# Performance work log

Hardware: AMD Instinct MI355X
Metric: run time of the kernel (lower is better)

Reference implementation:

```python
import jax, jax.numpy as jnp
from jax import lax
import numpy as np

B, T, F, H, O = 4096, 2048, 8, 32, 8


def setup_inputs() -> dict:
    key = jax.random.key(0)
    k = jax.random.split(key, 7)
    s = 1.0 / np.sqrt(H).astype(np.float32)  # torch RNN/Linear init bound
    x = jax.random.normal(k[0], (B, T, F), dtype=jnp.float32)
    W_ih = jax.random.uniform(k[1], (H, F), minval=-s, maxval=s, dtype=jnp.float32)
    W_hh = jax.random.uniform(k[2], (H, H), minval=-s, maxval=s, dtype=jnp.float32)
    b_ih = jax.random.uniform(k[3], (H,), minval=-s, maxval=s, dtype=jnp.float32)
    b_hh = jax.random.uniform(k[4], (H,), minval=-s, maxval=s, dtype=jnp.float32)
    W_out = jax.random.uniform(k[5], (O, H), minval=-s, maxval=s, dtype=jnp.float32)
    b_out = jax.random.uniform(k[6], (O,), minval=-s, maxval=s, dtype=jnp.float32)
    return {"x": x, "W_ih": W_ih, "W_hh": W_hh, "b_ih": b_ih, "b_hh": b_hh,
            "W_out": W_out, "b_out": b_out}


def reference(x, W_ih, W_hh, b_ih, b_hh, W_out, b_out):
    # Precompute input projection for all timesteps: [B, T, H]
    xp = jnp.einsum('btf,hf->bth', x, W_ih) + b_ih + b_hh
    h0 = jnp.zeros((x.shape[0], W_hh.shape[0]), dtype=x.dtype)

    def step(h, xt):  # xt: [B, H]
        h = jnp.tanh(xt + h @ W_hh.T)
        return h, None

    h_final, _ = lax.scan(step, h0, jnp.swapaxes(xp, 0, 1))  # scan over T
    # torch returns out(h) with h of shape [num_layers=1, B, H]
    y = h_final @ W_out.T + b_out  # [B, O]
    return y[None]  # [1, B, O]
```

## Files before the change

kernel.cpp:

```cpp
#include <hip/hip_runtime.h>


typedef float v2f __attribute__((ext_vector_type(2)));

static constexpr int T_STEPS = 2048;
static constexpr int FDIM    = 8;
static constexpr int HDIM    = 32;
static constexpr int ODIM    = 8;
static constexpr int WAVES_PER_BLOCK = 4;
static constexpr int GROUP   = 4;
static constexpr int NGROUP  = T_STEPS / GROUP;

__global__ __launch_bounds__(256, 4) void rnn_scan_kernel(
    const float* __restrict__ x,
    const float* __restrict__ W_ih,
    const float* __restrict__ W_hh,
    const float* __restrict__ b_ih,
    const float* __restrict__ b_hh,
    const float* __restrict__ W_out,
    const float* __restrict__ b_out,
    float* __restrict__ out)
{
    const float K = 2.8853900817779268f;
    const int tid  = threadIdx.x;
    const int lane = tid & 63;
    const int wave = tid >> 6;
    const int q    = lane & 31;
    const int half = lane >> 5;
    const long long b = (long long)blockIdx.x * WAVES_PER_BLOCK + wave;

    __shared__ float hsh[WAVES_PER_BLOCK][HDIM];

    v2f wh2[8];
    const float* whr = W_hh + q * HDIM + half * 16;
#pragma unroll
    for (int i = 0; i < 8; ++i) {
        v2f w; w[0] = whr[2 * i] * K; w[1] = whr[2 * i + 1] * K; wh2[i] = w;
    }
    v2f wi2[2];
    const float* wir = W_ih + q * FDIM + half * 4;
    {
        v2f w; w[0] = wir[0] * K; w[1] = wir[1] * K; wi2[0] = w;
        w[0] = wir[2] * K; w[1] = wir[3] * K; wi2[1] = w;
    }
    const float bias = half ? 0.0f : (b_ih[q] + b_hh[q]) * K;

    const int paddr = ((lane ^ 32) & 63) * 4;

    hsh[wave][q] = 0.0f;

    const float4* xq = reinterpret_cast<const float4*>(x + (size_t)b * T_STEPS * FDIM);
    const float4* hp = reinterpret_cast<const float4*>(&hsh[wave][half * 16]);
    float* hw = &hsh[wave][q];

    float4 cx0 = xq[0 + half], cx1 = xq[2 + half],
           cx2 = xq[4 + half], cx3 = xq[6 + half];

    for (int g = 0; g < NGROUP; ++g) {
        const int nb = ((g + 1 < NGROUP) ? (g + 1) : g) * (2 * GROUP);
        float4 nx0 = xq[nb + 0 + half], nx1 = xq[nb + 2 + half],
               nx2 = xq[nb + 4 + half], nx3 = xq[nb + 6 + half];
        asm volatile("" ::: "memory");

#define STEP(xr)                                                               \
        {                                                                      \
            float4 g0 = hp[0], g1 = hp[1], g2 = hp[2], g3 = hp[3];             \
            v2f a0; a0[0] = bias; a0[1] = 0.0f;                                \
            v2f a1; a1[0] = 0.0f; a1[1] = 0.0f;                                \
            v2f t2;                                                            \
            t2[0] = xr.x; t2[1] = xr.y;  a0 += wi2[0] * t2;                    \
            t2[0] = xr.z; t2[1] = xr.w;  a1 += wi2[1] * t2;                    \
            t2[0] = g0.x; t2[1] = g0.y;  a0 += wh2[0] * t2;                    \
            t2[0] = g0.z; t2[1] = g0.w;  a1 += wh2[1] * t2;                    \
            t2[0] = g1.x; t2[1] = g1.y;  a0 += wh2[2] * t2;                    \
            t2[0] = g1.z; t2[1] = g1.w;  a1 += wh2[3] * t2;                    \
            t2[0] = g2.x; t2[1] = g2.y;  a0 += wh2[4] * t2;                    \
            t2[0] = g2.z; t2[1] = g2.w;  a1 += wh2[5] * t2;                    \
            t2[0] = g3.x; t2[1] = g3.y;  a0 += wh2[6] * t2;                    \
            t2[0] = g3.z; t2[1] = g3.w;  a1 += wh2[7] * t2;                    \
            v2f as = a0 + a1;                                                  \
            float part = as[0] + as[1];                                        \
            float oth  = __int_as_float(__builtin_amdgcn_ds_bpermute(          \
                             paddr, __float_as_int(part)));                    \
            float s = part + oth;                                              \
            float e = __builtin_amdgcn_exp2f(s);                               \
            float r = __builtin_amdgcn_rcpf(e + 1.0f);                         \
            *hw = fmaf(-2.0f, r, 1.0f);                                        \
        }

        STEP(cx0) STEP(cx1) STEP(cx2) STEP(cx3)
#undef STEP

        cx0 = nx0; cx1 = nx1; cx2 = nx2; cx3 = nx3;
    }

    __syncthreads();
    if (tid < WAVES_PER_BLOCK * ODIM) {
        const int r = tid >> 3;
        const int o = tid & 7;
        float acc = b_out[o];
#pragma unroll
        for (int j = 0; j < HDIM; ++j)
            acc = fmaf(hsh[r][j], W_out[o * HDIM + j], acc);
        out[((long long)blockIdx.x * WAVES_PER_BLOCK + r) * ODIM + o] = acc;
    }
}

extern "C" void kernel_launch(void* const* d_in, const int* in_sizes, int n_in,
                              void* d_out, int out_size, void* d_ws, size_t ws_size,
                              hipStream_t stream) {
    const float* x     = (const float*)d_in[0];
    const float* W_ih  = (const float*)d_in[1];
    const float* W_hh  = (const float*)d_in[2];
    const float* b_ih  = (const float*)d_in[3];
    const float* b_hh  = (const float*)d_in[4];
    const float* W_out = (const float*)d_in[5];
    const float* b_out = (const float*)d_in[6];

    const int B = in_sizes[0] / (T_STEPS * FDIM);
    const int grid = B / WAVES_PER_BLOCK;

    rnn_scan_kernel<<<grid, 256, 0, stream>>>(
        x, W_ih, W_hh, b_ih, b_hh, W_out, b_out, (float*)d_out);
}
```

Before: 742.7 us.

## Map one batch row per half-wave, full 32-wide dot per lane

Each half-wave now owns one batch row, so every lane computes the full 32-element recurrent dot product instead of splitting it across two lanes. This removes the per-step ds_bpermute cross-lane reduction and doubles the rows per block to 8. The 8-element x rows are loaded through double-buffered register groups, and shared-memory rows are padded to a stride of 36 to spread LDS banks. Each lane now does twice the FMAs per step and holds more registers, with launch bounds reduced to 2 blocks per CU.

```diff
diff --git a/kernel.cpp b/kernel.cpp
--- a/kernel.cpp
+++ b/kernel.cpp
@@ -7,11 +7,12 @@
 static constexpr int FDIM    = 8;
 static constexpr int HDIM    = 32;
 static constexpr int ODIM    = 8;
-static constexpr int WAVES_PER_BLOCK = 4;
+static constexpr int ROWS_PER_BLOCK = 8;
 static constexpr int GROUP   = 4;
 static constexpr int NGROUP  = T_STEPS / GROUP;
+static constexpr int LSTR    = 36;
 
-__global__ __launch_bounds__(256, 4) void rnn_scan_kernel(
+__global__ __launch_bounds__(256, 2) void rnn_scan_kernel(
     const float* __restrict__ x,
     const float* __restrict__ W_ih,
     const float* __restrict__ W_hh,
@@ -26,83 +27,104 @@
     const int lane = tid & 63;
     const int wave = tid >> 6;
     const int q    = lane & 31;
-    const int half = lane >> 5;
-    const long long b = (long long)blockIdx.x * WAVES_PER_BLOCK + wave;
+    const int sub  = lane >> 5;
+    const int r    = wave * 2 + sub;
+    const long long b = (long long)blockIdx.x * ROWS_PER_BLOCK + r;
 
-    __shared__ float hsh[WAVES_PER_BLOCK][HDIM];
+    __shared__ float hsh[ROWS_PER_BLOCK][LSTR];
 
-    v2f wh2[8];
-    const float* whr = W_hh + q * HDIM + half * 16;
+    v2f wh[16];
+    const float* whr = W_hh + q * HDIM;
 #pragma unroll
-    for (int i = 0; i < 8; ++i) {
-        v2f w; w[0] = whr[2 * i] * K; w[1] = whr[2 * i + 1] * K; wh2[i] = w;
+    for (int i = 0; i < 16; ++i) {
+        v2f w; w[0] = whr[2 * i] * K; w[1] = whr[2 * i + 1] * K; wh[i] = w;
     }
-    v2f wi2[2];
-    const float* wir = W_ih + q * FDIM + half * 4;
-    {
-        v2f w; w[0] = wir[0] * K; w[1] = wir[1] * K; wi2[0] = w;
-        w[0] = wir[2] * K; w[1] = wir[3] * K; wi2[1] = w;
+    v2f wiv[4];
+    const float* wir = W_ih + q * FDIM;
+#pragma unroll
+    for (int i = 0; i < 4; ++i) {
+        v2f w; w[0] = wir[2 * i] * K; w[1] = wir[2 * i + 1] * K; wiv[i] = w;
     }
-    const float bias = half ? 0.0f : (b_ih[q] + b_hh[q]) * K;
+    const float bias = (b_ih[q] + b_hh[q]) * K;
 
-    const int paddr = ((lane ^ 32) & 63) * 4;
-
-    hsh[wave][q] = 0.0f;
+    hsh[r][q] = 0.0f;
 
     const float4* xq = reinterpret_cast<const float4*>(x + (size_t)b * T_STEPS * FDIM);
-    const float4* hp = reinterpret_cast<const float4*>(&hsh[wave][half * 16]);
-    float* hw = &hsh[wave][q];
+    const float4* hp = reinterpret_cast<const float4*>(&hsh[r][0]);
+    float* hw = &hsh[r][q];
 
-    float4 cx0 = xq[0 + half], cx1 = xq[2 + half],
-           cx2 = xq[4 + half], cx3 = xq[6 + half];
+#define LOADG(buf, gi)                                                         \
+    {                                                                          \
+        const int base = (gi) * (2 * GROUP);                                   \
+        _Pragma("unroll")                                                      \
+        for (int k = 0; k < 2 * GROUP; ++k) buf[k] = xq[base + k];             \
+    }                                                                          \
+    asm volatile("" ::: "memory");
 
-    for (int g = 0; g < NGROUP; ++g) {
-        const int nb = ((g + 1 < NGROUP) ? (g + 1) : g) * (2 * GROUP);
-        float4 nx0 = xq[nb + 0 + half], nx1 = xq[nb + 2 + half],
-               nx2 = xq[nb + 4 + half], nx3 = xq[nb + 6 + half];
-        asm volatile("" ::: "memory");
-
-#define STEP(xr)                                                               \
-        {                                                                      \
-            float4 g0 = hp[0], g1 = hp[1], g2 = hp[2], g3 = hp[3];             \
-            v2f a0; a0[0] = bias; a0[1] = 0.0f;                                \
-            v2f a1; a1[0] = 0.0f; a1[1] = 0.0f;                                \
-            v2f t2;                                                            \
-            t2[0] = xr.x; t2[1] = xr.y;  a0 += wi2[0] * t2;                    \
-            t2[0] = xr.z; t2[1] = xr.w;  a1 += wi2[1] * t2;                    \
-            t2[0] = g0.x; t2[1] = g0.y;  a0 += wh2[0] * t2;                    \
-            t2[0] = g0.z; t2[1] = g0.w;  a1 += wh2[1] * t2;                    \
-            t2[0] = g1.x; t2[1] = g1.y;  a0 += wh2[2] * t2;                    \
-            t2[0] = g1.z; t2[1] = g1.w;  a1 += wh2[3] * t2;                    \
-            t2[0] = g2.x; t2[1] = g2.y;  a0 += wh2[4] * t2;                    \
-            t2[0] = g2.z; t2[1] = g2.w;  a1 += wh2[5] * t2;                    \
-            t2[0] = g3.x; t2[1] = g3.y;  a0 += wh2[6] * t2;                    \
-            t2[0] = g3.z; t2[1] = g3.w;  a1 += wh2[7] * t2;                    \
-            v2f as = a0 + a1;                                                  \
-            float part = as[0] + as[1];                                        \
-            float oth  = __int_as_float(__builtin_amdgcn_ds_bpermute(          \
-                             paddr, __float_as_int(part)));                    \
-            float s = part + oth;                                              \
-            float e = __builtin_amdgcn_exp2f(s);                               \
-            float r = __builtin_amdgcn_rcpf(e + 1.0f);                         \
-            *hw = fmaf(-2.0f, r, 1.0f);                                        \
-        }
-
-        STEP(cx0) STEP(cx1) STEP(cx2) STEP(cx3)
-#undef STEP
-
-        cx0 = nx0; cx1 = nx1; cx2 = nx2; cx3 = nx3;
+#define STEP(xa, xb)                                                           \
+    {                                                                          \
+        float4 g0 = hp[0], g1 = hp[1], g2 = hp[2], g3 = hp[3];                 \
+        float4 g4 = hp[4], g5 = hp[5], g6 = hp[6], g7 = hp[7];                 \
+        v2f a0; a0[0] = bias; a0[1] = 0.0f;                                    \
+        v2f a1 = {0.0f, 0.0f}, a2 = {0.0f, 0.0f}, a3 = {0.0f, 0.0f};           \
+        v2f t;                                                                 \
+        t[0] = xa.x; t[1] = xa.y;  a0 = __builtin_elementwise_fma(wiv[0], t, a0); \
+        t[0] = xa.z; t[1] = xa.w;  a1 = __builtin_elementwise_fma(wiv[1], t, a1); \
+        t[0] = xb.x; t[1] = xb.y;  a2 = __builtin_elementwise_fma(wiv[2], t, a2); \
+        t[0] = xb.z; t[1] = xb.w;  a3 = __builtin_elementwise_fma(wiv[3], t, a3); \
+        t[0] = g0.x; t[1] = g0.y;  a0 = __builtin_elementwise_fma(wh[0],  t, a0); \
+        t[0] = g0.z; t[1] = g0.w;  a1 = __builtin_elementwise_fma(wh[1],  t, a1); \
+        t[0] = g1.x; t[1] = g1.y;  a2 = __builtin_elementwise_fma(wh[2],  t, a2); \
+        t[0] = g1.z; t[1] = g1.w;  a3 = __builtin_elementwise_fma(wh[3],  t, a3); \
+        t[0] = g2.x; t[1] = g2.y;  a0 = __builtin_elementwise_fma(wh[4],  t, a0); \
+        t[0] = g2.z; t[1] = g2.w;  a1 = __builtin_elementwise_fma(wh[5],  t, a1); \
+        t[0] = g3.x; t[1] = g3.y;  a2 = __builtin_elementwise_fma(wh[6],  t, a2); \
+        t[0] = g3.z; t[1] = g3.w;  a3 = __builtin_elementwise_fma(wh[7],  t, a3); \
+        t[0] = g4.x; t[1] = g4.y;  a0 = __builtin_elementwise_fma(wh[8],  t, a0); \
+        t[0] = g4.z; t[1] = g4.w;  a1 = __builtin_elementwise_fma(wh[9],  t, a1); \
+        t[0] = g5.x; t[1] = g5.y;  a2 = __builtin_elementwise_fma(wh[10], t, a2); \
+        t[0] = g5.z; t[1] = g5.w;  a3 = __builtin_elementwise_fma(wh[11], t, a3); \
+        t[0] = g6.x; t[1] = g6.y;  a0 = __builtin_elementwise_fma(wh[12], t, a0); \
+        t[0] = g6.z; t[1] = g6.w;  a1 = __builtin_elementwise_fma(wh[13], t, a1); \
+        t[0] = g7.x; t[1] = g7.y;  a2 = __builtin_elementwise_fma(wh[14], t, a2); \
+        t[0] = g7.z; t[1] = g7.w;  a3 = __builtin_elementwise_fma(wh[15], t, a3); \
+        v2f s01 = a0 + a1, s23 = a2 + a3;                                      \
+        v2f st  = s01 + s23;                                                   \
+        float s = st[0] + st[1];                                               \
+        float e = __builtin_amdgcn_exp2f(s);                                   \
+        float rc = __builtin_amdgcn_rcpf(e + 1.0f);                            \
+        *hw = fmaf(-2.0f, rc, 1.0f);                                           \
     }
 
+#define STEPS(buf)                                                             \
+    STEP(buf[0], buf[1]) STEP(buf[2], buf[3])                                  \
+    STEP(buf[4], buf[5]) STEP(buf[6], buf[7])
+
+    float4 bufA[2 * GROUP], bufB[2 * GROUP];
+    LOADG(bufA, 0)
+
+    for (int g = 0; g < NGROUP; g += 2) {
+        LOADG(bufB, g + 1)
+        STEPS(bufA)
+        {
+            const int gn = (g + 2 < NGROUP) ? (g + 2) : (NGROUP - 1);
+            LOADG(bufA, gn)
+        }
+        STEPS(bufB)
+    }
+#undef STEPS
+#undef STEP
+#undef LOADG
+
     __syncthreads();
-    if (tid < WAVES_PER_BLOCK * ODIM) {
-        const int r = tid >> 3;
-        const int o = tid & 7;
+    if (tid < ROWS_PER_BLOCK * ODIM) {
+        const int rr = tid >> 3;
+        const int o  = tid & 7;
         float acc = b_out[o];
 #pragma unroll
         for (int j = 0; j < HDIM; ++j)
-            acc = fmaf(hsh[r][j], W_out[o * HDIM + j], acc);
-        out[((long long)blockIdx.x * WAVES_PER_BLOCK + r) * ODIM + o] = acc;
+            acc = fmaf(hsh[rr][j], W_out[o * HDIM + j], acc);
+        out[((long long)blockIdx.x * ROWS_PER_BLOCK + rr) * ODIM + o] = acc;
     }
 }
 
@@ -118,7 +140,7 @@
     const float* b_out = (const float*)d_in[6];
 
     const int B = in_sizes[0] / (T_STEPS * FDIM);
-    const int grid = B / WAVES_PER_BLOCK;
+    const int grid = B / ROWS_PER_BLOCK;
 
     rnn_scan_kernel<<<grid, 256, 0, stream>>>(
         x, W_ih, W_hh, b_ih, b_hh, W_out, b_out, (float*)d_out);
```

New measurement: 687.0 us. 7.5% less time.
